# Kernel tuning notes

Measured on AMD Instinct MI355X. Metric: run time of the kernel, lower is better.

## Reference

```python
import jax, jax.numpy as jnp
import numpy as np

FILTER_WIDTH = 4  # w; output length = padded_length - w + 1


def setup_inputs() -> dict:
    key = jax.random.key(0)
    k1, k2 = jax.random.split(key)
    B, S, D = 256, 515, 512  # S = max_length + filter_width - 1
    x1 = jax.random.normal(k1, (B, 1, S, D), dtype=jnp.float32)
    x2 = jax.random.normal(k2, (B, 1, S, D), dtype=jnp.float32)
    return {"x1": x1, "x2": x2}


def _width_ap(x, vec, w):
    """ABCNN-2 attention-weighted window pooling.
    x: (B, 1, S, D), vec: (B, S) -> (B, 1, S - w + 1, D)
    out[:, :, j, :] = sum_{k=j}^{j+w-1} vec[:, k] * x[:, :, k, :]
    Implemented via cumulative sum for O(S*D) work.
    """
    weighted = x * vec[:, None, :, None]
    c = jnp.cumsum(weighted, axis=2)  # (B,1,S,D)
    S = x.shape[2]
    prev = jnp.concatenate([jnp.zeros_like(c[:, :, :1]), c[:, :, : S - w]], axis=2)
    return c[:, :, w - 1 :] - prev  # (B,1,S-w+1,D)


def reference(x1, x2):
    a = x1[:, 0]  # (B, S1, D)
    b = x2[:, 0]  # (B, S2, D)
    # pairwise squared euclidean distances via ||a||^2 + ||b||^2 - 2 a.b
    sq = (
        jnp.sum(a * a, axis=-1)[:, :, None]
        + jnp.sum(b * b, axis=-1)[:, None, :]
        - 2.0 * jnp.einsum("bid,bjd->bij", a, b)
    )
    A = 1.0 / (1.0 + jnp.sqrt(jnp.maximum(sq, 0.0)))  # (B, S1, S2)
    x1_vec = A.sum(axis=2)  # (B, S1) row sums
    x2_vec = A.sum(axis=1)  # (B, S2) col sums
    w1 = _width_ap(x1, x1_vec, FILTER_WIDTH)
    w2 = _width_ap(x2, x2_vec, FILTER_WIDTH)
    return (w1, w2)
```

## Files before the change

### kernel.cpp

```cpp
#include <hip/hip_runtime.h>
#include <hip/hip_bf16.h>

#define BATCH 256
#define SEQ   515
#define DIM   512
#define SOUT  512
#define BS_   (BATCH*SEQ)

#define BM 128
#define BK 64
#define NT 5

typedef float  f32x4  __attribute__((ext_vector_type(4)));
typedef __bf16 bf16x8 __attribute__((ext_vector_type(8)));

__device__ inline unsigned int pack2(float a, float b) {
  unsigned short ua = __builtin_bit_cast(unsigned short, (__bf16)a);
  unsigned short ub = __builtin_bit_cast(unsigned short, (__bf16)b);
  return (unsigned int)ua | ((unsigned int)ub << 16);
}

__device__ inline void gload_lds16(const void* g, void* l) {
  __builtin_amdgcn_global_load_lds(
      (const __attribute__((address_space(1))) unsigned int*)g,
      (__attribute__((address_space(3))) unsigned int*)l, 16, 0, 0);
}

__device__ inline float fastA(float sq) {
  float t = __builtin_amdgcn_sqrtf(fmaxf(sq, 0.f));
  return __builtin_amdgcn_rcpf(1.f + t);
}

__global__ __launch_bounds__(256) void convert_norms_kernel(
    const float* __restrict__ x1, const float* __restrict__ x2,
    unsigned short* __restrict__ x1b, unsigned short* __restrict__ x2b,
    float* __restrict__ nrm) {
  int wid  = blockIdx.x * 4 + (threadIdx.x >> 6);
  int lane = threadIdx.x & 63;
  if (wid >= 2 * BS_) return;
  bool second = wid >= BS_;
  int r = second ? wid - BS_ : wid;
  const float4* p = (const float4*)((second ? x2 : x1) + (size_t)r * DIM) + lane * 2;
  float4 a = p[0];
  float4 b = p[1];
  uint4 wv;
  wv.x = pack2(a.x, a.y); wv.y = pack2(a.z, a.w);
  wv.z = pack2(b.x, b.y); wv.w = pack2(b.z, b.w);
  *((uint4*)((second ? x2b : x1b) + (size_t)r * DIM) + lane) = wv;
  float s = a.x*a.x + a.y*a.y + a.z*a.z + a.w*a.w
          + b.x*b.x + b.y*b.y + b.z*b.z + b.w*b.w;
#pragma unroll
  for (int m = 1; m < 64; m <<= 1) s += __shfl_xor(s, m, 64);
  if (lane == 0) nrm[wid] = s;
}

__global__ __launch_bounds__(512, 2) void gemm_batch_kernel(
    const unsigned short* __restrict__ xab, const unsigned short* __restrict__ xbb,
    const float* __restrict__ nrm,
    float* __restrict__ v1, float* __restrict__ v2) {
  const int b    = blockIdx.x;
  const int tid  = threadIdx.x;
  const int lane = tid & 63, w = tid >> 6;
  const int wr   = w >> 2, wc = w & 3;

  __shared__ alignas(16) unsigned char As[2][256 * 128];
  __shared__ alignas(16) unsigned char Bs[2][256 * 128];
  __shared__ float v1acc[512];
  __shared__ float v2acc[512];
  __shared__ float nals[512];
  __shared__ float nbls[512];
  __shared__ alignas(16) unsigned short t1ls[4][512];
  __shared__ alignas(16) unsigned short t2ls[4][512];
  __shared__ float nt1s[4], nt2s[4], t1sum[4], t2sum[4];

  const char* aB = (const char*)(xab + (size_t)b * SEQ * DIM);
  const char* bB = (const char*)(xbb + (size_t)b * SEQ * DIM);

  v1acc[tid] = 0.f;
  v2acc[tid] = 0.f;
  nals[tid] = nrm[b * SEQ + tid];
  nbls[tid] = nrm[BS_ + b * SEQ + tid];
  {
    int rr = tid >> 7;
    int cc = (tid & 127) * 4;
    uint2 d1 = {0u, 0u}, d2 = {0u, 0u};
    if (rr < 3) {
      d1 = *(const uint2*)(aB + (size_t)(512 + rr) * 1024 + cc * 2);
      d2 = *(const uint2*)(bB + (size_t)(512 + rr) * 1024 + cc * 2);
    }
    *(uint2*)&t1ls[rr][cc] = d1;
    *(uint2*)&t2ls[rr][cc] = d2;
  }
  if (tid < 3) {
    nt1s[tid] = nrm[b * SEQ + 512 + tid];
    nt2s[tid] = nrm[BS_ + b * SEQ + 512 + tid];
    t1sum[tid] = 0.f; t2sum[tid] = 0.f;
  }

  const int l3       = lane >> 3;
  const int laneByte = ((lane & 7) ^ l3) * 16;

  const int arow = wr * 128 + (lane & 15);
  const int brow = wc * 64  + (lane & 15);

  const char* t1base = (const char*)t1ls + (lane & 3) * 1024;
  const char* t2base = (const char*)t2ls + (lane & 3) * 1024;

  f32x4 acc[8][4] = {};
  f32x4 acc_t1[4] = {};
  f32x4 acc_t2[8] = {};
  f32x4 acc_t3 = {};

  auto STAGE = [&](int s, unsigned char* pa, unsigned char* pb) {
    const int t = s >> 3;
    const int tiN = t >> 1, tjN = (t & 1) ^ (t >> 1), ktN = (s & 7) * BK;
#pragma unroll
    for (int i = 0; i < 4; ++i) {
      int u = w * 4 + i;
      gload_lds16(aB + (size_t)(tiN * 256 + u * 8 + l3) * 1024 + ktN * 2 + laneByte,
                  pa + u * 1024);
      gload_lds16(bB + (size_t)(tjN * 256 + u * 8 + l3) * 1024 + ktN * 2 + laneByte,
                  pb + u * 1024);
    }
  };

  STAGE(0, As[0], Bs[0]);

#pragma unroll 1
  for (int s = 0; s < 32; ++s) {
    asm volatile("s_waitcnt vmcnt(0)" ::: "memory");
    __builtin_amdgcn_s_barrier();
    if (s < 31) STAGE(s + 1, As[(s + 1) & 1], Bs[(s + 1) & 1]);

    const int t  = s >> 3;
    const int ti = t >> 1, tj = (t & 1) ^ (t >> 1);
    const bool gT1 = (wr == 0) && (ti == 0);
    const bool gT2 = (wc == 0) && (tj == 0);
    const bool gT3 = (w == 0) && (t == 0);

    const unsigned char* Ac = As[s & 1];
    const unsigned char* Bc = Bs[s & 1];
#pragma unroll
    for (int ks = 0; ks < 2; ++ks) {
      const int xorterm = ((ks * 4 + (lane >> 4)) ^ (lane & 7)) * 16;
      const int koff = ((s & 7) * 64 + ks * 32 + ((lane >> 4) << 3)) * 2;
      bf16x8 t1f = {}, t2f = {};
      if (gT1 || gT3) t1f = *(const bf16x8*)(t1base + koff);
      if (gT2 || gT3) t2f = *(const bf16x8*)(t2base + koff);
      bf16x8 bfv[4];
#pragma unroll
      for (int f = 0; f < 4; ++f)
        bfv[f] = *(const bf16x8*)(Bc + (brow + f * 16) * 128 + xorterm);
      if (gT1) {
#pragma unroll
        for (int f = 0; f < 4; ++f)
          acc_t1[f] = __builtin_amdgcn_mfma_f32_16x16x32_bf16(t1f, bfv[f], acc_t1[f], 0, 0, 0);
      }
      if (gT3)
        acc_t3 = __builtin_amdgcn_mfma_f32_16x16x32_bf16(t1f, t2f, acc_t3, 0, 0, 0);
#pragma unroll
      for (int fi = 0; fi < 8; ++fi) {
        bf16x8 af = *(const bf16x8*)(Ac + (arow + fi * 16) * 128 + xorterm);
#pragma unroll
        for (int fj = 0; fj < 4; ++fj)
          acc[fi][fj] = __builtin_amdgcn_mfma_f32_16x16x32_bf16(
              af, bfv[fj], acc[fi][fj], 0, 0, 0);
        if (gT2)
          acc_t2[fi] = __builtin_amdgcn_mfma_f32_16x16x32_bf16(af, t2f, acc_t2[fi], 0, 0, 0);
      }
    }

    if ((s & 7) == 7) {
      const int ibase = ti * 256 + wr * 128;
      const int jbase = tj * 256 + wc * 64;

      float cs[4] = {0.f, 0.f, 0.f, 0.f};
      int   gj[4]; float nbv[4];
#pragma unroll
      for (int fj = 0; fj < 4; ++fj) {
        gj[fj]  = jbase + fj * 16 + (lane & 15);
        nbv[fj] = nbls[gj[fj]];
      }
#pragma unroll
      for (int fi = 0; fi < 8; ++fi) {
        int r0 = ibase + fi * 16 + ((lane >> 4) << 2);
#pragma unroll
        for (int reg = 0; reg < 4; ++reg) {
          float nav = nals[r0 + reg];
          float sps = 0.f;
#pragma unroll
          for (int fj = 0; fj < 4; ++fj) {
            float Aij = fastA(nav + nbv[fj] - 2.f * acc[fi][fj][reg]);
            sps += Aij;
            cs[fj] += Aij;
          }
          sps += __shfl_xor(sps, 1);  sps += __shfl_xor(sps, 2);
          sps += __shfl_xor(sps, 4);  sps += __shfl_xor(sps, 8);
          if ((lane & 15) == 0) atomicAdd(&v1acc[r0 + reg], sps);
        }
      }
#pragma unroll
      for (int fj = 0; fj < 4; ++fj) {
        float sv = cs[fj];
        sv += __shfl_xor(sv, 16); sv += __shfl_xor(sv, 32);
        if (lane < 16) atomicAdd(&v2acc[gj[fj]], sv);
      }
#pragma unroll
      for (int fi = 0; fi < 8; ++fi)
#pragma unroll
        for (int fj = 0; fj < 4; ++fj)
          acc[fi][fj] = (f32x4){0.f, 0.f, 0.f, 0.f};

      if (gT1) {
        float p0 = 0.f, p1 = 0.f, p2 = 0.f;
#pragma unroll
        for (int f = 0; f < 4; ++f) {
          if (lane < 16) {
            int j = jbase + f * 16 + lane;
            float A0 = fastA(nt1s[0] + nbls[j] - 2.f * acc_t1[f][0]);
            float A1 = fastA(nt1s[1] + nbls[j] - 2.f * acc_t1[f][1]);
            float A2 = fastA(nt1s[2] + nbls[j] - 2.f * acc_t1[f][2]);
            atomicAdd(&v2acc[j], A0 + A1 + A2);
            p0 += A0; p1 += A1; p2 += A2;
          }
          acc_t1[f] = (f32x4){0.f, 0.f, 0.f, 0.f};
        }
        p0 += __shfl_xor(p0, 1); p0 += __shfl_xor(p0, 2);
        p0 += __shfl_xor(p0, 4); p0 += __shfl_xor(p0, 8);
        p1 += __shfl_xor(p1, 1); p1 += __shfl_xor(p1, 2);
        p1 += __shfl_xor(p1, 4); p1 += __shfl_xor(p1, 8);
        p2 += __shfl_xor(p2, 1); p2 += __shfl_xor(p2, 2);
        p2 += __shfl_xor(p2, 4); p2 += __shfl_xor(p2, 8);
        if (lane == 0) {
          atomicAdd(&t1sum[0], p0);
          atomicAdd(&t1sum[1], p1);
          atomicAdd(&t1sum[2], p2);
        }
      }

      if (gT2) {
        float q = 0.f;
        const int colv = lane & 15;
        float ntc = (colv < 3) ? nt2s[colv] : 0.f;
#pragma unroll
        for (int fi = 0; fi < 8; ++fi) {
          if (colv < 3) {
            int i0 = ibase + fi * 16 + ((lane >> 4) << 2);
#pragma unroll
            for (int e = 0; e < 4; ++e) {
              float Av = fastA(ntc + nals[i0 + e] - 2.f * acc_t2[fi][e]);
              atomicAdd(&v1acc[i0 + e], Av);
              q += Av;
            }
          }
          acc_t2[fi] = (f32x4){0.f, 0.f, 0.f, 0.f};
        }
        q += __shfl_xor(q, 16); q += __shfl_xor(q, 32);
        if (lane < 3) atomicAdd(&t2sum[lane], q);
      }

      if (gT3) {
        if (lane < 3) {
#pragma unroll
          for (int e = 0; e < 3; ++e) {
            float Av = fastA(nt1s[e] + nt2s[lane] - 2.f * acc_t3[e]);
            atomicAdd(&t1sum[e], Av);
            atomicAdd(&t2sum[lane], Av);
          }
        }
        acc_t3 = (f32x4){0.f, 0.f, 0.f, 0.f};
      }
    }
  }
  __syncthreads();

  v1[b * SEQ + tid] = v1acc[tid];
  v2[b * SEQ + tid] = v2acc[tid];
  if (tid < 3) {
    v1[b * SEQ + 512 + tid] = t1sum[tid];
    v2[b * SEQ + 512 + tid] = t2sum[tid];
  }
}

__global__ __launch_bounds__(128) void pool_bf16_kernel(
    const unsigned short* __restrict__ x1b, const unsigned short* __restrict__ x2b,
    const float* __restrict__ v1, const float* __restrict__ v2,
    float* __restrict__ out) {
  const int t     = threadIdx.x;
  const int chunk = blockIdx.x;
  const int b     = blockIdx.y;
  const int which = blockIdx.z;
  const unsigned short* x = which ? x2b : x1b;
  const float*        vec = which ? v2 : v1;
  float4* o = (float4*)out + (size_t)which * ((size_t)BATCH * SOUT * DIM / 4);
  const ushort4* xr = (const ushort4*)(x + (size_t)b * SEQ * DIM);
  const float*   vb = vec + b * SEQ;
  const int j0 = chunk * 64;

  float4 r0 = {0,0,0,0}, r1 = {0,0,0,0}, r2 = {0,0,0,0}, r3 = {0,0,0,0};
#pragma unroll 1
  for (int g = 0; g < 17; ++g) {
#pragma unroll
    for (int u = 0; u < 4; ++u) {
      int kk = g * 4 + u;
      int k  = j0 + kk;
      float4 val = {0,0,0,0};
      if (k < SEQ) {
        float   w  = vb[k];
        ushort4 xv = xr[(size_t)k * 128 + t];
        val.x = w * (float)__builtin_bit_cast(__bf16, (unsigned short)xv.x);
        val.y = w * (float)__builtin_bit_cast(__bf16, (unsigned short)xv.y);
        val.z = w * (float)__builtin_bit_cast(__bf16, (unsigned short)xv.z);
        val.w = w * (float)__builtin_bit_cast(__bf16, (unsigned short)xv.w);
      }
      if      (u == 0) r0 = val;
      else if (u == 1) r1 = val;
      else if (u == 2) r2 = val;
      else             r3 = val;
      if (kk >= 3 && kk <= 66) {
        int jout = k - 3;
        float4 sum;
        sum.x = r0.x + r1.x + r2.x + r3.x;
        sum.y = r0.y + r1.y + r2.y + r3.y;
        sum.z = r0.z + r1.z + r2.z + r3.z;
        sum.w = r0.w + r1.w + r2.w + r3.w;
        o[((size_t)b * SOUT + jout) * 128 + t] = sum;
      }
    }
  }
}

__global__ __launch_bounds__(256) void norms_kernel(
    const float* __restrict__ x1, const float* __restrict__ x2,
    float* __restrict__ nrm) {
  int wid  = blockIdx.x * 4 + (threadIdx.x >> 6);
  int lane = threadIdx.x & 63;
  if (wid >= 2 * BS_) return;
  const float* base = (wid < BS_) ? x1 : x2;
  int r = (wid < BS_) ? wid : wid - BS_;
  const float4* p = (const float4*)(base + (size_t)r * DIM);
  float4 a = p[lane];
  float4 b = p[lane + 64];
  float s = a.x*a.x + a.y*a.y + a.z*a.z + a.w*a.w
          + b.x*b.x + b.y*b.y + b.z*b.z + b.w*b.w;
#pragma unroll
  for (int m = 1; m < 64; m <<= 1) s += __shfl_xor(s, m, 64);
  if (lane == 0) nrm[wid] = s;
}

__global__ __launch_bounds__(256) void attn_sums_kernel(
    const float* __restrict__ x1, const float* __restrict__ x2,
    const float* __restrict__ nrm,
    float* __restrict__ v1, float* __restrict__ v2) {
  const int b   = blockIdx.y;
  const int ti  = blockIdx.x / NT, tj = blockIdx.x % NT;
  const int tid = threadIdx.x;
  const int lane = tid & 63, wid = tid >> 6;
  const int wr = wid >> 1, wc = wid & 1;

  __shared__ alignas(16) unsigned char AsB[BM * BK * 2];
  __shared__ alignas(16) unsigned char BsB[BM * BK * 2];

  const float* aB = x1 + (size_t)b * SEQ * DIM;
  const float* bB = x2 + (size_t)b * SEQ * DIM;

  f32x4 acc[4][4] = {};
  const int rloc = tid >> 4;
  const int c4   = tid & 15;

  for (int kt = 0; kt < DIM; kt += BK) {
#pragma unroll
    for (int p = 0; p < 8; ++p) {
      int r = p * 16 + rloc;
      int wroff = r * 128 + ((c4 * 8) ^ ((r & 7) << 4));
      int gra = ti * BM + r;
      float4 va = make_float4(0.f, 0.f, 0.f, 0.f);
      if (gra < SEQ) va = *(const float4*)(aB + (size_t)gra * DIM + kt + c4 * 4);
      uint2 wa; wa.x = pack2(va.x, va.y); wa.y = pack2(va.z, va.w);
      *(uint2*)(AsB + wroff) = wa;
      int grb = tj * BM + r;
      float4 vb = make_float4(0.f, 0.f, 0.f, 0.f);
      if (grb < SEQ) vb = *(const float4*)(bB + (size_t)grb * DIM + kt + c4 * 4);
      uint2 wb; wb.x = pack2(vb.x, vb.y); wb.y = pack2(vb.z, vb.w);
      *(uint2*)(BsB + wroff) = wb;
    }
    __syncthreads();
#pragma unroll
    for (int ks = 0; ks < 2; ++ks) {
      bf16x8 af[4], bfv[4];
      int kb = ks * 64 + ((lane >> 4) << 4);
#pragma unroll
      for (int f = 0; f < 4; ++f) {
        int ar = wr * 64 + f * 16 + (lane & 15);
        af[f]  = *(const bf16x8*)(AsB + ar * 128 + (kb ^ ((ar & 7) << 4)));
        int br = wc * 64 + f * 16 + (lane & 15);
        bfv[f] = *(const bf16x8*)(BsB + br * 128 + (kb ^ ((br & 7) << 4)));
      }
#pragma unroll
      for (int fi = 0; fi < 4; ++fi)
#pragma unroll
        for (int fj = 0; fj < 4; ++fj)
          acc[fi][fj] = __builtin_amdgcn_mfma_f32_16x16x32_bf16(
              af[fi], bfv[fj], acc[fi][fj], 0, 0, 0);
    }
    __syncthreads();
  }

  const float* na = nrm;
  const float* nb = nrm + BS_;
  const int ibase = ti * BM + wr * 64;
  const int jbase = tj * BM + wc * 64;

  float cs[4] = {0.f, 0.f, 0.f, 0.f};
  int   gj[4]; float nbv[4]; bool jv[4];
#pragma unroll
  for (int fj = 0; fj < 4; ++fj) {
    gj[fj]  = jbase + fj * 16 + (lane & 15);
    jv[fj]  = gj[fj] < SEQ;
    nbv[fj] = jv[fj] ? nb[b * SEQ + gj[fj]] : 0.f;
  }
#pragma unroll
  for (int fi = 0; fi < 4; ++fi) {
    int r0 = ibase + fi * 16 + ((lane >> 4) << 2);
    float rs[4];
#pragma unroll
    for (int reg = 0; reg < 4; ++reg) {
      int gi = r0 + reg;
      bool iv = gi < SEQ;
      float nav = iv ? na[b * SEQ + gi] : 0.f;
      float s = 0.f;
#pragma unroll
      for (int fj = 0; fj < 4; ++fj) {
        float c  = acc[fi][fj][reg];
        float sq = nav + nbv[fj] - 2.f * c;
        float Aij = (iv && jv[fj]) ? 1.f / (1.f + sqrtf(fmaxf(sq, 0.f))) : 0.f;
        s += Aij;
        cs[fj] += Aij;
      }
      rs[reg] = s;
    }
#pragma unroll
    for (int reg = 0; reg < 4; ++reg) {
      float s = rs[reg];
      s += __shfl_xor(s, 1);  s += __shfl_xor(s, 2);
      s += __shfl_xor(s, 4);  s += __shfl_xor(s, 8);
      int gi = r0 + reg;
      if ((lane & 15) == 0 && gi < SEQ) atomicAdd(&v1[b * SEQ + gi], s);
    }
  }
#pragma unroll
  for (int fj = 0; fj < 4; ++fj) {
    float s = cs[fj];
    s += __shfl_xor(s, 16); s += __shfl_xor(s, 32);
    if (lane < 16 && jv[fj]) atomicAdd(&v2[b * SEQ + gj[fj]], s);
  }
}

__global__ __launch_bounds__(128) void pool_kernel(
    const float* __restrict__ x1, const float* __restrict__ x2,
    const float* __restrict__ v1, const float* __restrict__ v2,
    float* __restrict__ out) {
  const int t     = threadIdx.x;
  const int chunk = blockIdx.x;
  const int b     = blockIdx.y;
  const int which = blockIdx.z;
  const float*  x   = which ? x2 : x1;
  const float*  vec = which ? v2 : v1;
  float4* o = (float4*)out + (size_t)which * ((size_t)BATCH * SOUT * DIM / 4);
  const float4* xr = (const float4*)(x + (size_t)b * SEQ * DIM);
  const float*  vb = vec + b * SEQ;
  const int j0 = chunk * 64;

  float4 r0 = {0,0,0,0}, r1 = {0,0,0,0}, r2 = {0,0,0,0}, r3 = {0,0,0,0};
#pragma unroll 1
  for (int g = 0; g < 17; ++g) {
#pragma unroll
    for (int u = 0; u < 4; ++u) {
      int kk = g * 4 + u;
      int k  = j0 + kk;
      float4 val = {0,0,0,0};
      if (k < SEQ) {
        float  w  = vb[k];
        float4 xv = xr[(size_t)k * 128 + t];
        val.x = w * xv.x; val.y = w * xv.y; val.z = w * xv.z; val.w = w * xv.w;
      }
      if      (u == 0) r0 = val;
      else if (u == 1) r1 = val;
      else if (u == 2) r2 = val;
      else             r3 = val;
      if (kk >= 3 && kk <= 66) {
        int jout = k - 3;
        float4 sum;
        sum.x = r0.x + r1.x + r2.x + r3.x;
        sum.y = r0.y + r1.y + r2.y + r3.y;
        sum.z = r0.z + r1.z + r2.z + r3.z;
        sum.w = r0.w + r1.w + r2.w + r3.w;
        o[((size_t)b * SOUT + jout) * 128 + t] = sum;
      }
    }
  }
}

extern "C" void kernel_launch(void* const* d_in, const int* in_sizes, int n_in,
                              void* d_out, int out_size, void* d_ws, size_t ws_size,
                              hipStream_t stream) {
  const float* x1 = (const float*)d_in[0];
  const float* x2 = (const float*)d_in[1];
  float* out = (float*)d_out;
  float* ws  = (float*)d_ws;
  float* nrm = ws;
  float* v1  = ws + 2 * BS_;
  float* v2  = ws + 3 * BS_;

  const size_t need = (size_t)4 * BS_ * sizeof(float)
                    + (size_t)2 * BS_ * DIM * sizeof(unsigned short);

  if (ws_size >= need) {
    unsigned short* x1b = (unsigned short*)(ws + 4 * BS_);
    unsigned short* x2b = x1b + (size_t)BS_ * DIM;
    convert_norms_kernel<<<(2 * BS_ + 3) / 4, 256, 0, stream>>>(x1, x2, x1b, x2b, nrm);
    gemm_batch_kernel<<<BATCH, 512, 0, stream>>>(x1b, x2b, nrm, v1, v2);
    pool_bf16_kernel<<<dim3(8, BATCH, 2), 128, 0, stream>>>(x1b, x2b, v1, v2, out);
  } else {
    hipMemsetAsync(v1, 0, 2 * (size_t)BS_ * sizeof(float), stream);
    norms_kernel<<<(2 * BS_ + 3) / 4, 256, 0, stream>>>(x1, x2, nrm);
    attn_sums_kernel<<<dim3(NT * NT, BATCH), 256, 0, stream>>>(x1, x2, nrm, v1, v2);
    pool_kernel<<<dim3(8, BATCH, 2), 128, 0, stream>>>(x1, x2, v1, v2, out);
  }
}
```

Before: 467.3 us.

## Fuse window pooling into batched GEMM kernel epilogue

Removes the separate pooling kernel and does the attention-weighted window pooling at the end of the per-batch GEMM block. The row and column sums are read straight from shared memory instead of going through global memory, and one kernel launch is saved. In exchange, each of the 256 blocks now does the whole pooling for its batch serially over both sides with 512 threads. This cuts parallelism relative to the previous 4096-block pooling grid and may leave the memory-bound phase underutilising the GPU.

```diff
diff --git a/kernel.cpp b/kernel.cpp
--- a/kernel.cpp
+++ b/kernel.cpp
@@ -56,8 +56,7 @@
 
 __global__ __launch_bounds__(512, 2) void gemm_batch_kernel(
     const unsigned short* __restrict__ xab, const unsigned short* __restrict__ xbb,
-    const float* __restrict__ nrm,
-    float* __restrict__ v1, float* __restrict__ v2) {
+    const float* __restrict__ nrm, float* __restrict__ out) {
   const int b    = blockIdx.x;
   const int tid  = threadIdx.x;
   const int lane = tid & 63, w = tid >> 6;
@@ -274,57 +273,45 @@
   }
   __syncthreads();
 
-  v1[b * SEQ + tid] = v1acc[tid];
-  v2[b * SEQ + tid] = v2acc[tid];
-  if (tid < 3) {
-    v1[b * SEQ + 512 + tid] = t1sum[tid];
-    v2[b * SEQ + 512 + tid] = t2sum[tid];
-  }
-}
-
-__global__ __launch_bounds__(128) void pool_bf16_kernel(
-    const unsigned short* __restrict__ x1b, const unsigned short* __restrict__ x2b,
-    const float* __restrict__ v1, const float* __restrict__ v2,
-    float* __restrict__ out) {
-  const int t     = threadIdx.x;
-  const int chunk = blockIdx.x;
-  const int b     = blockIdx.y;
-  const int which = blockIdx.z;
-  const unsigned short* x = which ? x2b : x1b;
-  const float*        vec = which ? v2 : v1;
-  float4* o = (float4*)out + (size_t)which * ((size_t)BATCH * SOUT * DIM / 4);
-  const ushort4* xr = (const ushort4*)(x + (size_t)b * SEQ * DIM);
-  const float*   vb = vec + b * SEQ;
-  const int j0 = chunk * 64;
-
-  float4 r0 = {0,0,0,0}, r1 = {0,0,0,0}, r2 = {0,0,0,0}, r3 = {0,0,0,0};
+  const int rg  = tid >> 7;
+  const int col = tid & 127;
+  const int j0  = rg * 128;
 #pragma unroll 1
-  for (int g = 0; g < 17; ++g) {
-#pragma unroll
-    for (int u = 0; u < 4; ++u) {
-      int kk = g * 4 + u;
-      int k  = j0 + kk;
-      float4 val = {0,0,0,0};
-      if (k < SEQ) {
-        float   w  = vb[k];
-        ushort4 xv = xr[(size_t)k * 128 + t];
-        val.x = w * (float)__builtin_bit_cast(__bf16, (unsigned short)xv.x);
-        val.y = w * (float)__builtin_bit_cast(__bf16, (unsigned short)xv.y);
-        val.z = w * (float)__builtin_bit_cast(__bf16, (unsigned short)xv.z);
-        val.w = w * (float)__builtin_bit_cast(__bf16, (unsigned short)xv.w);
-      }
-      if      (u == 0) r0 = val;
-      else if (u == 1) r1 = val;
-      else if (u == 2) r2 = val;
-      else             r3 = val;
-      if (kk >= 3 && kk <= 66) {
-        int jout = k - 3;
-        float4 sum;
-        sum.x = r0.x + r1.x + r2.x + r3.x;
-        sum.y = r0.y + r1.y + r2.y + r3.y;
-        sum.z = r0.z + r1.z + r2.z + r3.z;
-        sum.w = r0.w + r1.w + r2.w + r3.w;
-        o[((size_t)b * SOUT + jout) * 128 + t] = sum;
+  for (int side = 0; side < 2; ++side) {
+    const unsigned short* xb = (side ? xbb : xab) + (size_t)b * SEQ * DIM;
+    const float* vsrc = side ? v2acc : v1acc;
+    const float* tsrc = side ? t2sum : t1sum;
+    float* ob = out + (size_t)side * ((size_t)BATCH * SOUT * DIM)
+                    + (size_t)b * SOUT * DIM;
+    float4 r0 = {0,0,0,0}, r1 = r0, r2 = r0, r3 = r0;
+#pragma unroll 1
+    for (int g = 0; g < 33; ++g) {
+#pragma unroll
+      for (int u = 0; u < 4; ++u) {
+        int kk = g * 4 + u;
+        int k  = j0 + kk;
+        float4 val = {0,0,0,0};
+        if (kk < 131 && k < SEQ) {
+          float w = (k < 512) ? vsrc[k] : tsrc[k - 512];
+          uint2 xv = *(const uint2*)(xb + (size_t)k * DIM + col * 4);
+          val.x = w * __builtin_bit_cast(float, xv.x << 16);
+          val.y = w * __builtin_bit_cast(float, xv.x & 0xffff0000u);
+          val.z = w * __builtin_bit_cast(float, xv.y << 16);
+          val.w = w * __builtin_bit_cast(float, xv.y & 0xffff0000u);
+        }
+        if      (u == 0) r0 = val;
+        else if (u == 1) r1 = val;
+        else if (u == 2) r2 = val;
+        else             r3 = val;
+        if (kk >= 3 && kk <= 130) {
+          int j = k - 3;
+          float4 sum;
+          sum.x = r0.x + r1.x + r2.x + r3.x;
+          sum.y = r0.y + r1.y + r2.y + r3.y;
+          sum.z = r0.z + r1.z + r2.z + r3.z;
+          sum.w = r0.w + r1.w + r2.w + r3.w;
+          *(float4*)(ob + (size_t)j * DIM + col * 4) = sum;
+        }
       }
     }
   }
@@ -519,8 +506,7 @@
     unsigned short* x1b = (unsigned short*)(ws + 4 * BS_);
     unsigned short* x2b = x1b + (size_t)BS_ * DIM;
     convert_norms_kernel<<<(2 * BS_ + 3) / 4, 256, 0, stream>>>(x1, x2, x1b, x2b, nrm);
-    gemm_batch_kernel<<<BATCH, 512, 0, stream>>>(x1b, x2b, nrm, v1, v2);
-    pool_bf16_kernel<<<dim3(8, BATCH, 2), 128, 0, stream>>>(x1b, x2b, v1, v2, out);
+    gemm_batch_kernel<<<BATCH, 512, 0, stream>>>(x1b, x2b, nrm, out);
   } else {
     hipMemsetAsync(v1, 0, 2 * (size_t)BS_ * sizeof(float), stream);
     norms_kernel<<<(2 * BS_ + 3) / 4, 256, 0, stream>>>(x1, x2, nrm);
```

New measurement: 543.6 us. +16.3%, slower.
